# Kernel tuning notes

Hardware: AMD Instinct MI355X
Metric: run time of the kernel (lower is better)

## Reference

```python
import jax, jax.numpy as jnp
import numpy as np

N_QUBITS = 18
LAYERS = 6
DATA_REUPLOADING = True


def _apply_1q(state, gate, q, n):
    # state: [2^n] complex, gate: [2,2] complex, acts on qubit q (big-endian)
    s = state.reshape(2 ** q, 2, 2 ** (n - q - 1))
    s = jnp.einsum('ab,ibj->iaj', gate, s)
    return s.reshape(-1)


def _apply_cz_adj(state, q, n):
    # CZ on adjacent qubits (q, q+1): flip sign of |..11..> amplitudes
    s = state.reshape(2 ** q, 2, 2, 2 ** (n - q - 2))
    s = s.at[:, 1, 1, :].multiply(-1.0)
    return s.reshape(-1)


def _rx(t):
    c = jnp.cos(t / 2).astype(jnp.complex64)
    s = (-1j * jnp.sin(t / 2)).astype(jnp.complex64)
    return jnp.stack([jnp.stack([c, s]), jnp.stack([s, c])])


def _ry(t):
    c = jnp.cos(t / 2).astype(jnp.complex64)
    s = jnp.sin(t / 2).astype(jnp.complex64)
    return jnp.stack([jnp.stack([c, -s]), jnp.stack([s, c])])


def _rz(t):
    em = jnp.exp(-1j * t.astype(jnp.complex64) / 2)
    ep = jnp.exp(1j * t.astype(jnp.complex64) / 2)
    z = jnp.zeros((), jnp.complex64)
    return jnp.stack([jnp.stack([em, z]), jnp.stack([z, ep])])


def _circuit(x, input_scaling, variational):
    # Hardware-efficient ansatz: RX(data) encoding, RY+RZ variational, CZ chain
    n = N_QUBITS
    state = jnp.zeros(2 ** n, jnp.complex64).at[0].set(1.0)
    for l in range(LAYERS):
        if l == 0 or DATA_REUPLOADING:
            for q in range(n):
                state = _apply_1q(state, _rx(input_scaling[l, q] * x[q]), q, n)
        for q in range(n):
            state = _apply_1q(state, _ry(variational[l, q]), q, n)
        for q in range(n):
            state = _apply_1q(state, _rz(variational[l, n + q]), q, n)
        for q in range(n - 1):
            state = _apply_cz_adj(state, q, n)
    return state


def setup_inputs() -> dict:
    key = jax.random.key(0)
    k1, k2, k3 = jax.random.split(key, 3)
    x1 = jax.random.normal(k1, (N_QUBITS,), jnp.float32)
    x2 = jax.random.normal(k2, (N_QUBITS,), jnp.float32)
    input_scaling = jnp.ones((LAYERS, N_QUBITS), jnp.float32)
    variational = (jax.random.uniform(k3, (LAYERS, 2 * N_QUBITS), jnp.float32)
                   * 2 * np.pi - np.pi)
    return {"x1": x1, "x2": x2, "input_scaling": input_scaling,
            "variational": variational}


def reference(x1, x2, input_scaling, variational):
    psi1 = _circuit(x1, input_scaling, variational)
    psi2 = _circuit(x2, input_scaling, variational)
    # projector |0><0| expectation of U(x2)^dagger U(x1)|0> == |<psi2|psi1>|^2
    ov = jnp.vdot(psi2, psi1)
    return (ov.real ** 2 + ov.imag ** 2).astype(jnp.float32)
```

## Files before the change

### kernel.cpp

```cpp
#include <hip/hip_runtime.h>
#include <math.h>


#define NQ      18
#define NSTATE  (1 << NQ)
#define TPB     256
#define MAGIC   0x5EED5EEDu

__device__ __forceinline__ int SW(int i) { return i ^ ((i >> 5) & 31); }

__device__ __forceinline__ float2 cmulf(float2 a, float2 b) {
    return make_float2(a.x * b.x - a.y * b.y, a.x * b.y + a.y * b.x);
}

__device__ __forceinline__ float lxor(float x, int j) {
    if (j == 0) {
        int v = __float_as_int(x);
        return __int_as_float(__builtin_amdgcn_update_dpp(v, v, 0xB1, 0xF, 0xF, false));
    }
    if (j == 1) {
        int v = __float_as_int(x);
        return __int_as_float(__builtin_amdgcn_update_dpp(v, v, 0x4E, 0xF, 0xF, false));
    }
    return __shfl_xor(x, 1 << j, 64);
}

__device__ __forceinline__ void cpair(
    float& a0r, float& a0i, float& a1r, float& a1i,
    float u00r, float u00i, float u01r, float u01i,
    float u10r, float u10i, float u11r, float u11i)
{
    float n0r = u00r * a0r - u00i * a0i + u01r * a1r - u01i * a1i;
    float n0i = u00r * a0i + u00i * a0r + u01r * a1i + u01i * a1r;
    float n1r = u10r * a0r - u10i * a0i + u11r * a1r - u11i * a1i;
    float n1i = u10r * a0i + u10i * a0r + u11r * a1i + u11i * a1r;
    a0r = n0r; a0i = n0i; a1r = n1r; a1i = n1i;
}

template<int RB>
__device__ __forceinline__ void reg_gate8(float (&ar)[8], float (&ai)[8],
                                          const float2* up)
{
    float u00r = up[0].x, u00i = up[0].y, u01r = up[1].x, u01i = up[1].y;
    float u10r = up[2].x, u10i = up[2].y, u11r = up[3].x, u11i = up[3].y;
#pragma unroll
    for (int r = 0; r < 8; ++r) {
        if (r & RB) continue;
        int r1 = r | RB;
        cpair(ar[r], ai[r], ar[r1], ai[r1],
              u00r, u00i, u01r, u01i, u10r, u10i, u11r, u11i);
    }
}

__device__ __forceinline__ void lane_gate8(float (&ar)[8], float (&ai)[8],
                                           const float2* up, int lane, int j)
{
    float u00r = up[0].x, u00i = up[0].y, u01r = up[1].x, u01i = up[1].y;
    float u10r = up[2].x, u10i = up[2].y, u11r = up[3].x, u11i = up[3].y;
    int side = (lane >> j) & 1;
    float car = side ? u11r : u00r, cai = side ? u11i : u00i;
    float cbr = side ? u10r : u01r, cbi = side ? u10i : u01i;
#pragma unroll
    for (int r = 0; r < 8; ++r) {
        float pr = lxor(ar[r], j);
        float pi = lxor(ai[r], j);
        float mr = ar[r], mi = ai[r];
        ar[r] = car * mr - cai * mi + cbr * pr - cbi * pi;
        ai[r] = car * mi + cai * mr + cbr * pi + cbi * pr;
    }
}

__global__ __launch_bounds__(TPB) void sim_kernel(
    float2* __restrict__ states,
    const float* __restrict__ x1, const float* __restrict__ x2,
    const float* __restrict__ iscale, const float* __restrict__ var,
    double* __restrict__ acc, unsigned* __restrict__ cnt,
    unsigned* __restrict__ flags, float* __restrict__ out)
{
    __shared__ float sre[2048], sim_[2048];
    __shared__ float2 sUa[5 * 11 * 4];
    __shared__ float2 sUb[5 * 11 * 4];
    __shared__ float2 sDa[6 * 4];
    __shared__ float2 sDb[11 * 4];
    __shared__ double wr[4], wi[4];

    int blk = blockIdx.x, t = threadIdx.x, lane = t & 63, wave = t >> 6;
    int c = blk >> 7, gc = blk & 127;
    const float* xv = c ? x2 : x1;

    if (blk == 0 && t == 0) {
        acc[0] = 0.0; acc[1] = 0.0; *cnt = 0u;
        __hip_atomic_store(&flags[128 * 16], MAGIC, __ATOMIC_RELEASE,
                           __HIP_MEMORY_SCOPE_AGENT);
    }

    if (t < 110) {
        int which = t >= 55;
        int tt = which ? t - 55 : t;
        int l = tt / 11, w = tt % 11;
        int q = which ? (17 - w) : (10 - w);
        float tx = iscale[l * NQ + q] * xv[q];
        float ty = var[l * 2 * NQ + q];
        float tz = var[l * 2 * NQ + NQ + q];
        float sx, cx, sy, cy, sz, cz;
        sincosf(tx * 0.5f, &sx, &cx);
        sincosf(ty * 0.5f, &sy, &cy);
        sincosf(tz * 0.5f, &sz, &cz);
        float m00r = cy * cx,  m00i =  sy * sx;
        float m01r = -sy * cx, m01i = -cy * sx;
        float m10r = sy * cx,  m10i = -cy * sx;
        float m11r = cy * cx,  m11i = -sy * sx;
        float2* up = which ? &sUb[(l * 11 + w) * 4] : &sUa[(l * 11 + w) * 4];
        up[0] = make_float2(m00r * cz + m00i * sz, m00i * cz - m00r * sz);
        up[1] = make_float2(m01r * cz + m01i * sz, m01i * cz - m01r * sz);
        up[2] = make_float2(m10r * cz - m10i * sz, m10i * cz + m10r * sz);
        up[3] = make_float2(m11r * cz - m11i * sz, m11i * cz + m11r * sz);
    } else if (t < 127) {
        int isb = t >= 116;
        int j = isb ? (t - 116) : (t - 110);
        int q = isb ? (17 - j) : (5 - j);
        float d = iscale[5 * NQ + q] * (x1[q] - x2[q]);
        float sn, cs;
        sincosf(d * 0.5f, &sn, &cs);
        float2* up = isb ? &sDb[j * 4] : &sDa[j * 4];
        up[0] = make_float2(cs, 0.f);  up[1] = make_float2(0.f, sn);
        up[2] = make_float2(0.f, sn);  up[3] = make_float2(cs, 0.f);
    }
    __syncthreads();

    float ar[8], ai[8];
    auto W1 = [&](int r) { return r | (wave << 3) | (lane << 5); };
    auto W2 = [&](int r) { return wave | (r << 2) | (lane << 5); };
    auto X1 = [&](int r) { return lane | (wave << 6) | (r << 8); };
    auto X2 = [&](int r) { return lane | (r << 6) | (wave << 9); };
    auto rot = [&](auto from, auto to) {
#pragma unroll
        for (int r = 0; r < 8; ++r) { int s = SW(from(r)); sre[s] = ar[r]; sim_[s] = ai[r]; }
        __syncthreads();
#pragma unroll
        for (int r = 0; r < 8; ++r) { int s = SW(to(r)); ar[r] = sre[s]; ai[r] = sim_[s]; }
    };
    auto Ua = [&](int l, int w) -> const float2* { return &sUa[(l * 11 + w) * 4]; };
    auto Ub = [&](int l, int w) -> const float2* { return &sUb[(l * 11 + w) * 4]; };
    auto czfold = [&](unsigned M, auto gidx) {
#pragma unroll
        for (int r = 0; r < 8; ++r) {
            int i = gidx(r);
            if (__popc(i & (i >> 1) & M) & 1) { ar[r] = -ar[r]; ai[r] = -ai[r]; }
        }
    };
    auto g1_1 = [&](int r) { return W1(r) << 7; };
    auto g1_2 = [&](int r) { return W2(r) << 7; };
    auto g2_1 = [&](int r) { return (gc << 11) | X1(r); };
    auto g2_2 = [&](int r) { return (gc << 11) | X2(r); };

    {
        float2 com = make_float2(1.f, 0.f);
        const float2* u3 = Ua(0, 3); com = cmulf(com, (wave & 1) ? u3[2] : u3[0]);
        const float2* u4 = Ua(0, 4); com = cmulf(com, (wave >> 1) ? u4[2] : u4[0]);
#pragma unroll
        for (int j = 0; j < 6; ++j) {
            const float2* u = Ua(0, 5 + j);
            com = cmulf(com, ((lane >> j) & 1) ? u[2] : u[0]);
        }
        const float2* u0 = Ua(0, 0); const float2* u1 = Ua(0, 1); const float2* u2 = Ua(0, 2);
#pragma unroll
        for (int r = 0; r < 8; ++r) {
            float2 f = cmulf((r & 1) ? u0[2] : u0[0], (r & 2) ? u1[2] : u1[0]);
            f = cmulf(f, (r & 4) ? u2[2] : u2[0]);
            f = cmulf(com, f);
            ar[r] = f.x; ai[r] = f.y;
        }
    }
    czfold(0x1FF80u, g1_1);
    reg_gate8<2>(ar, ai, Ua(1, 1));
    reg_gate8<4>(ar, ai, Ua(1, 2));
#pragma unroll
    for (int j = 0; j < 6; ++j) lane_gate8(ar, ai, Ua(1, 5 + j), lane, j);
    rot(W1, W2);
    reg_gate8<2>(ar, ai, Ua(1, 3));
    reg_gate8<4>(ar, ai, Ua(1, 4));
    czfold(0x1FF00u, g1_2);
    reg_gate8<1>(ar, ai, Ua(2, 2));
    reg_gate8<2>(ar, ai, Ua(2, 3));
    reg_gate8<4>(ar, ai, Ua(2, 4));
#pragma unroll
    for (int j = 0; j < 6; ++j) lane_gate8(ar, ai, Ua(2, 5 + j), lane, j);
    rot(W2, W1);
    czfold(0x1FE00u, g1_1);
#pragma unroll
    for (int j = 0; j < 6; ++j) lane_gate8(ar, ai, Ua(3, 5 + j), lane, j);
    rot(W1, W2);
    reg_gate8<2>(ar, ai, Ua(3, 3));
    reg_gate8<4>(ar, ai, Ua(3, 4));
    czfold(0x1FC00u, g1_2);
    reg_gate8<4>(ar, ai, Ua(4, 4));
#pragma unroll
    for (int j = 0; j < 6; ++j) lane_gate8(ar, ai, Ua(4, 5 + j), lane, j);
    rot(W2, W1);
    czfold(0x1F800u, g1_1);
    if (c == 1) {
#pragma unroll
        for (int j = 0; j < 6; ++j) lane_gate8(ar, ai, &sDa[j * 4], lane, j);
    }
#pragma unroll
    for (int r = 0; r < 8; ++r) { int s = SW(W1(r)); sre[s] = ar[r]; sim_[s] = ai[r]; }
    __syncthreads();
#pragma unroll
    for (int r = 0; r < 8; ++r) {
        int x = X1(r);
        if ((x & 127) == 0) {
            int Wv = (gc << 4) | (x >> 7);
            int s = SW(Wv);
            ar[r] = sre[s]; ai[r] = sim_[s];
        } else { ar[r] = 0.f; ai[r] = 0.f; }
    }
    __syncthreads();

#pragma unroll
    for (int j = 0; j < 6; ++j) lane_gate8(ar, ai, Ub(0, j), lane, j);
    rot(X1, X2);
    reg_gate8<1>(ar, ai, Ub(0, 6));
    czfold(0x7Fu, g2_2);
#pragma unroll
    for (int j = 0; j < 6; ++j) lane_gate8(ar, ai, Ub(1, j), lane, j);
    reg_gate8<1>(ar, ai, Ub(1, 6));
    reg_gate8<2>(ar, ai, Ub(1, 7));
    rot(X2, X1);
    czfold(0xFFu, g2_1);
#pragma unroll
    for (int j = 0; j < 6; ++j) lane_gate8(ar, ai, Ub(2, j), lane, j);
    reg_gate8<1>(ar, ai, Ub(2, 8));
    rot(X1, X2);
    reg_gate8<1>(ar, ai, Ub(2, 6));
    reg_gate8<2>(ar, ai, Ub(2, 7));
    czfold(0x1FFu, g2_2);
#pragma unroll
    for (int j = 0; j < 6; ++j) lane_gate8(ar, ai, Ub(3, j), lane, j);
    reg_gate8<1>(ar, ai, Ub(3, 6));
    reg_gate8<2>(ar, ai, Ub(3, 7));
    reg_gate8<4>(ar, ai, Ub(3, 8));
    rot(X2, X1);
    reg_gate8<2>(ar, ai, Ub(3, 9));
    czfold(0x3FFu, g2_1);
#pragma unroll
    for (int j = 0; j < 6; ++j) lane_gate8(ar, ai, Ub(4, j), lane, j);
    reg_gate8<1>(ar, ai, Ub(4, 8));
    reg_gate8<2>(ar, ai, Ub(4, 9));
    reg_gate8<4>(ar, ai, Ub(4, 10));
    czfold(0x71Fu, g2_1);
    if (c == 1) {
#pragma unroll
        for (int j = 0; j < 5; ++j) lane_gate8(ar, ai, &sDb[j * 4], lane, j);
        reg_gate8<2>(ar, ai, &sDb[9 * 4]);
        reg_gate8<4>(ar, ai, &sDb[10 * 4]);
    }
    rot(X1, X2);
    reg_gate8<1>(ar, ai, Ub(4, 6));
    reg_gate8<2>(ar, ai, Ub(4, 7));
    czfold(0xE0u, g2_2);

    if (c == 0) {
#pragma unroll
        for (int r = 0; r < 8; ++r) {
            int i = (gc << 11) | X2(r);
            states[i] = make_float2(ar[r], ai[r]);
        }
        __syncthreads();
        if (t == 0) {
            __hip_atomic_store(&flags[gc * 16], MAGIC, __ATOMIC_RELEASE,
                               __HIP_MEMORY_SCOPE_AGENT);
        }
    } else {
        lane_gate8(ar, ai, &sDb[5 * 4], lane, 5);
        reg_gate8<1>(ar, ai, &sDb[6 * 4]);
        reg_gate8<2>(ar, ai, &sDb[7 * 4]);
        reg_gate8<4>(ar, ai, &sDb[8 * 4]);

        float d6 = iscale[5 * NQ + 6] * (x1[6] - x2[6]);
        float sn6, cs6;
        sincosf(d6 * 0.5f, &sn6, &cs6);
        float cf = cs6, sf = sn6;

        if (t == 0) {
            while (__hip_atomic_load(&flags[gc * 16], __ATOMIC_RELAXED,
                                     __HIP_MEMORY_SCOPE_AGENT) != MAGIC)
                __builtin_amdgcn_s_sleep(1);
            while (__hip_atomic_load(&flags[(gc ^ 1) * 16], __ATOMIC_RELAXED,
                                     __HIP_MEMORY_SCOPE_AGENT) != MAGIC)
                __builtin_amdgcn_s_sleep(1);
            while (__hip_atomic_load(&flags[128 * 16], __ATOMIC_RELAXED,
                                     __HIP_MEMORY_SCOPE_AGENT) != MAGIC)
                __builtin_amdgcn_s_sleep(1);
            __builtin_amdgcn_fence(__ATOMIC_ACQUIRE, "agent");
        }
        __syncthreads();

        double accr = 0.0, acci = 0.0;
#pragma unroll
        for (int r = 0; r < 8; ++r) {
            int i = (gc << 11) | X2(r);
            float2 p1 = states[i];
            float2 pp = states[i ^ 2048];
            float gr = cf * p1.x + sf * pp.y;
            float gi = cf * p1.y - sf * pp.x;
            accr += (double)ar[r] * gr + (double)ai[r] * gi;
            acci += (double)ar[r] * gi - (double)ai[r] * gr;
        }
        for (int o = 32; o > 0; o >>= 1) {
            accr += __shfl_down(accr, o, 64);
            acci += __shfl_down(acci, o, 64);
        }
        if (lane == 0) { wr[wave] = accr; wi[wave] = acci; }
        __syncthreads();
        if (t == 0) {
            double br = wr[0] + wr[1] + wr[2] + wr[3];
            double bi = wi[0] + wi[1] + wi[2] + wi[3];
            atomicAdd(&acc[0], br);
            atomicAdd(&acc[1], bi);
            __threadfence();
            unsigned old = atomicAdd(cnt, 1u);
            if (old == 127u) {
                double fr = atomicAdd(&acc[0], 0.0);
                double fi = atomicAdd(&acc[1], 0.0);
                out[0] = (float)(fr * fr + fi * fi);
            }
        }
    }
}

extern "C" void kernel_launch(void* const* d_in, const int* in_sizes, int n_in,
                              void* d_out, int out_size, void* d_ws, size_t ws_size,
                              hipStream_t stream)
{
    const float* x1 = (const float*)d_in[0];
    const float* x2 = (const float*)d_in[1];
    const float* iscale = (const float*)d_in[2];
    const float* var = (const float*)d_in[3];
    float* out = (float*)d_out;

    double*   acc    = (double*)((char*)d_ws + 8192);
    unsigned* cnt    = (unsigned*)((char*)d_ws + 8320);
    unsigned* flags  = (unsigned*)((char*)d_ws + 16384);
    float2*   states = (float2*)((char*)d_ws + 65536);

    sim_kernel<<<256, TPB, 0, stream>>>(states, x1, x2, iscale, var,
                                        acc, cnt, flags, out);
}
```

Measured before the change: 93.06 us.

## Double threads per block, halving per-thread register amplitudes

Raises block size from 256 to 512 threads so each thread holds 4 amplitudes instead of 8. The register-index and wave-bit mappings are redesigned, and the gate schedule and LDS rotations are reordered to suit the new layouts. A second barrier is added inside each rotation, and extra rotations are inserted near the end. The aim is more parallelism and latency hiding per block on a fixed grid of 256 blocks, at the cost of more barriers and LDS traffic per amplitude.

```diff
diff --git a/kernel.cpp b/kernel.cpp
--- a/kernel.cpp
+++ b/kernel.cpp
@@ -4,7 +4,7 @@
 
 #define NQ      18
 #define NSTATE  (1 << NQ)
-#define TPB     256
+#define TPB     512
 #define MAGIC   0x5EED5EEDu
 
 __device__ __forceinline__ int SW(int i) { return i ^ ((i >> 5) & 31); }
@@ -38,13 +38,13 @@
 }
 
 template<int RB>
-__device__ __forceinline__ void reg_gate8(float (&ar)[8], float (&ai)[8],
+__device__ __forceinline__ void reg_gate4(float (&ar)[4], float (&ai)[4],
                                           const float2* up)
 {
     float u00r = up[0].x, u00i = up[0].y, u01r = up[1].x, u01i = up[1].y;
     float u10r = up[2].x, u10i = up[2].y, u11r = up[3].x, u11i = up[3].y;
 #pragma unroll
-    for (int r = 0; r < 8; ++r) {
+    for (int r = 0; r < 4; ++r) {
         if (r & RB) continue;
         int r1 = r | RB;
         cpair(ar[r], ai[r], ar[r1], ai[r1],
@@ -52,7 +52,7 @@
     }
 }
 
-__device__ __forceinline__ void lane_gate8(float (&ar)[8], float (&ai)[8],
+__device__ __forceinline__ void lane_gate4(float (&ar)[4], float (&ai)[4],
                                            const float2* up, int lane, int j)
 {
     float u00r = up[0].x, u00i = up[0].y, u01r = up[1].x, u01i = up[1].y;
@@ -61,7 +61,7 @@
     float car = side ? u11r : u00r, cai = side ? u11i : u00i;
     float cbr = side ? u10r : u01r, cbi = side ? u10i : u01i;
 #pragma unroll
-    for (int r = 0; r < 8; ++r) {
+    for (int r = 0; r < 4; ++r) {
         float pr = lxor(ar[r], j);
         float pi = lxor(ai[r], j);
         float mr = ar[r], mi = ai[r];
@@ -82,10 +82,11 @@
     __shared__ float2 sUb[5 * 11 * 4];
     __shared__ float2 sDa[6 * 4];
     __shared__ float2 sDb[11 * 4];
-    __shared__ double wr[4], wi[4];
+    __shared__ double wr[8], wi[8];
 
     int blk = blockIdx.x, t = threadIdx.x, lane = t & 63, wave = t >> 6;
     int c = blk >> 7, gc = blk & 127;
+    int wv0 = wave & 1, wv1 = (wave >> 1) & 1, wv2 = (wave >> 2) & 1;
     const float* xv = c ? x2 : x1;
 
     if (blk == 0 && t == 0) {
@@ -128,87 +129,100 @@
     }
     __syncthreads();
 
-    float ar[8], ai[8];
-    auto W1 = [&](int r) { return r | (wave << 3) | (lane << 5); };
-    auto W2 = [&](int r) { return wave | (r << 2) | (lane << 5); };
-    auto X1 = [&](int r) { return lane | (wave << 6) | (r << 8); };
-    auto X2 = [&](int r) { return lane | (r << 6) | (wave << 9); };
+    float ar[4], ai[4];
+    auto V1 = [&](int r) { return wv0 | ((r & 1) << 1) | (((r >> 1) & 1) << 2)
+                                | (wv1 << 3) | (wv2 << 4) | (lane << 5); };
+    auto V2 = [&](int r) { return wv0 | (wv1 << 1) | (wv2 << 2)
+                                | ((r & 1) << 3) | (((r >> 1) & 1) << 4) | (lane << 5); };
+    auto V3 = [&](int r) { return wv0 | (wv1 << 1) | ((r & 1) << 2)
+                                | (((r >> 1) & 1) << 3) | (wv2 << 4) | (lane << 5); };
+    auto T1 = [&](int r) { return lane | ((r & 1) << 6) | (((r >> 1) & 1) << 7)
+                                | (wv0 << 8) | (wv1 << 9) | (wv2 << 10); };
+    auto T2 = [&](int r) { return lane | (wv0 << 6) | (wv1 << 7)
+                                | ((r & 1) << 8) | (((r >> 1) & 1) << 9) | (wv2 << 10); };
+    auto T6 = [&](int r) { return lane | (wv0 << 6) | (wv1 << 7) | (wv2 << 8)
+                                | ((r & 1) << 9) | (((r >> 1) & 1) << 10); };
+    auto T8 = [&](int r) { return lane | (wv0 << 6) | (wv1 << 7)
+                                | ((r & 1) << 8) | (wv2 << 9) | (((r >> 1) & 1) << 10); };
     auto rot = [&](auto from, auto to) {
 #pragma unroll
-        for (int r = 0; r < 8; ++r) { int s = SW(from(r)); sre[s] = ar[r]; sim_[s] = ai[r]; }
-        __syncthreads();
-#pragma unroll
-        for (int r = 0; r < 8; ++r) { int s = SW(to(r)); ar[r] = sre[s]; ai[r] = sim_[s]; }
+        for (int r = 0; r < 4; ++r) { int s = SW(from(r)); sre[s] = ar[r]; sim_[s] = ai[r]; }
+        __syncthreads();
+#pragma unroll
+        for (int r = 0; r < 4; ++r) { int s = SW(to(r)); ar[r] = sre[s]; ai[r] = sim_[s]; }
+        __syncthreads();
     };
     auto Ua = [&](int l, int w) -> const float2* { return &sUa[(l * 11 + w) * 4]; };
     auto Ub = [&](int l, int w) -> const float2* { return &sUb[(l * 11 + w) * 4]; };
     auto czfold = [&](unsigned M, auto gidx) {
 #pragma unroll
-        for (int r = 0; r < 8; ++r) {
+        for (int r = 0; r < 4; ++r) {
             int i = gidx(r);
             if (__popc(i & (i >> 1) & M) & 1) { ar[r] = -ar[r]; ai[r] = -ai[r]; }
         }
     };
-    auto g1_1 = [&](int r) { return W1(r) << 7; };
-    auto g1_2 = [&](int r) { return W2(r) << 7; };
-    auto g2_1 = [&](int r) { return (gc << 11) | X1(r); };
-    auto g2_2 = [&](int r) { return (gc << 11) | X2(r); };
+    auto gV1 = [&](int r) { return V1(r) << 7; };
+    auto gV2 = [&](int r) { return V2(r) << 7; };
+    auto gV3 = [&](int r) { return V3(r) << 7; };
+    auto gT1 = [&](int r) { return (gc << 11) | T1(r); };
+    auto gT2 = [&](int r) { return (gc << 11) | T2(r); };
+    auto gT6 = [&](int r) { return (gc << 11) | T6(r); };
 
     {
         float2 com = make_float2(1.f, 0.f);
-        const float2* u3 = Ua(0, 3); com = cmulf(com, (wave & 1) ? u3[2] : u3[0]);
-        const float2* u4 = Ua(0, 4); com = cmulf(com, (wave >> 1) ? u4[2] : u4[0]);
+        const float2* u0 = Ua(0, 0); com = cmulf(com, wv0 ? u0[2] : u0[0]);
+        const float2* u3 = Ua(0, 3); com = cmulf(com, wv1 ? u3[2] : u3[0]);
+        const float2* u4 = Ua(0, 4); com = cmulf(com, wv2 ? u4[2] : u4[0]);
 #pragma unroll
         for (int j = 0; j < 6; ++j) {
             const float2* u = Ua(0, 5 + j);
             com = cmulf(com, ((lane >> j) & 1) ? u[2] : u[0]);
         }
-        const float2* u0 = Ua(0, 0); const float2* u1 = Ua(0, 1); const float2* u2 = Ua(0, 2);
-#pragma unroll
-        for (int r = 0; r < 8; ++r) {
-            float2 f = cmulf((r & 1) ? u0[2] : u0[0], (r & 2) ? u1[2] : u1[0]);
-            f = cmulf(f, (r & 4) ? u2[2] : u2[0]);
+        const float2* u1 = Ua(0, 1); const float2* u2 = Ua(0, 2);
+#pragma unroll
+        for (int r = 0; r < 4; ++r) {
+            float2 f = cmulf((r & 1) ? u1[2] : u1[0], (r & 2) ? u2[2] : u2[0]);
             f = cmulf(com, f);
             ar[r] = f.x; ai[r] = f.y;
         }
     }
-    czfold(0x1FF80u, g1_1);
-    reg_gate8<2>(ar, ai, Ua(1, 1));
-    reg_gate8<4>(ar, ai, Ua(1, 2));
-#pragma unroll
-    for (int j = 0; j < 6; ++j) lane_gate8(ar, ai, Ua(1, 5 + j), lane, j);
-    rot(W1, W2);
-    reg_gate8<2>(ar, ai, Ua(1, 3));
-    reg_gate8<4>(ar, ai, Ua(1, 4));
-    czfold(0x1FF00u, g1_2);
-    reg_gate8<1>(ar, ai, Ua(2, 2));
-    reg_gate8<2>(ar, ai, Ua(2, 3));
-    reg_gate8<4>(ar, ai, Ua(2, 4));
-#pragma unroll
-    for (int j = 0; j < 6; ++j) lane_gate8(ar, ai, Ua(2, 5 + j), lane, j);
-    rot(W2, W1);
-    czfold(0x1FE00u, g1_1);
-#pragma unroll
-    for (int j = 0; j < 6; ++j) lane_gate8(ar, ai, Ua(3, 5 + j), lane, j);
-    rot(W1, W2);
-    reg_gate8<2>(ar, ai, Ua(3, 3));
-    reg_gate8<4>(ar, ai, Ua(3, 4));
-    czfold(0x1FC00u, g1_2);
-    reg_gate8<4>(ar, ai, Ua(4, 4));
-#pragma unroll
-    for (int j = 0; j < 6; ++j) lane_gate8(ar, ai, Ua(4, 5 + j), lane, j);
-    rot(W2, W1);
-    czfold(0x1F800u, g1_1);
+    czfold(0x1FF80u, gV1);
+    reg_gate4<1>(ar, ai, Ua(1, 1));
+    reg_gate4<2>(ar, ai, Ua(1, 2));
+#pragma unroll
+    for (int j = 0; j < 6; ++j) lane_gate4(ar, ai, Ua(1, 5 + j), lane, j);
+    rot(V1, V2);
+    reg_gate4<1>(ar, ai, Ua(1, 3));
+    reg_gate4<2>(ar, ai, Ua(1, 4));
+    czfold(0x1FF00u, gV2);
+    reg_gate4<1>(ar, ai, Ua(2, 3));
+    reg_gate4<2>(ar, ai, Ua(2, 4));
+#pragma unroll
+    for (int j = 0; j < 6; ++j) lane_gate4(ar, ai, Ua(2, 5 + j), lane, j);
+    rot(V2, V3);
+    reg_gate4<1>(ar, ai, Ua(2, 2));
+    czfold(0x1FE00u, gV3);
+    reg_gate4<2>(ar, ai, Ua(3, 3));
+#pragma unroll
+    for (int j = 0; j < 6; ++j) lane_gate4(ar, ai, Ua(3, 5 + j), lane, j);
+    rot(V3, V2);
+    reg_gate4<2>(ar, ai, Ua(3, 4));
+    czfold(0x1FC00u, gV2);
+    reg_gate4<2>(ar, ai, Ua(4, 4));
+#pragma unroll
+    for (int j = 0; j < 6; ++j) lane_gate4(ar, ai, Ua(4, 5 + j), lane, j);
+    rot(V2, V1);
+    czfold(0x1F800u, gV1);
     if (c == 1) {
 #pragma unroll
-        for (int j = 0; j < 6; ++j) lane_gate8(ar, ai, &sDa[j * 4], lane, j);
-    }
-#pragma unroll
-    for (int r = 0; r < 8; ++r) { int s = SW(W1(r)); sre[s] = ar[r]; sim_[s] = ai[r]; }
+        for (int j = 0; j < 6; ++j) lane_gate4(ar, ai, &sDa[j * 4], lane, j);
+    }
+#pragma unroll
+    for (int r = 0; r < 4; ++r) { int s = SW(V1(r)); sre[s] = ar[r]; sim_[s] = ai[r]; }
     __syncthreads();
 #pragma unroll
-    for (int r = 0; r < 8; ++r) {
-        int x = X1(r);
+    for (int r = 0; r < 4; ++r) {
+        int x = T1(r);
         if ((x & 127) == 0) {
             int Wv = (gc << 4) | (x >> 7);
             int s = SW(Wv);
@@ -218,52 +232,46 @@
     __syncthreads();
 
 #pragma unroll
-    for (int j = 0; j < 6; ++j) lane_gate8(ar, ai, Ub(0, j), lane, j);
-    rot(X1, X2);
-    reg_gate8<1>(ar, ai, Ub(0, 6));
-    czfold(0x7Fu, g2_2);
-#pragma unroll
-    for (int j = 0; j < 6; ++j) lane_gate8(ar, ai, Ub(1, j), lane, j);
-    reg_gate8<1>(ar, ai, Ub(1, 6));
-    reg_gate8<2>(ar, ai, Ub(1, 7));
-    rot(X2, X1);
-    czfold(0xFFu, g2_1);
-#pragma unroll
-    for (int j = 0; j < 6; ++j) lane_gate8(ar, ai, Ub(2, j), lane, j);
-    reg_gate8<1>(ar, ai, Ub(2, 8));
-    rot(X1, X2);
-    reg_gate8<1>(ar, ai, Ub(2, 6));
-    reg_gate8<2>(ar, ai, Ub(2, 7));
-    czfold(0x1FFu, g2_2);
-#pragma unroll
-    for (int j = 0; j < 6; ++j) lane_gate8(ar, ai, Ub(3, j), lane, j);
-    reg_gate8<1>(ar, ai, Ub(3, 6));
-    reg_gate8<2>(ar, ai, Ub(3, 7));
-    reg_gate8<4>(ar, ai, Ub(3, 8));
-    rot(X2, X1);
-    reg_gate8<2>(ar, ai, Ub(3, 9));
-    czfold(0x3FFu, g2_1);
-#pragma unroll
-    for (int j = 0; j < 6; ++j) lane_gate8(ar, ai, Ub(4, j), lane, j);
-    reg_gate8<1>(ar, ai, Ub(4, 8));
-    reg_gate8<2>(ar, ai, Ub(4, 9));
-    reg_gate8<4>(ar, ai, Ub(4, 10));
-    czfold(0x71Fu, g2_1);
-    if (c == 1) {
-#pragma unroll
-        for (int j = 0; j < 5; ++j) lane_gate8(ar, ai, &sDb[j * 4], lane, j);
-        reg_gate8<2>(ar, ai, &sDb[9 * 4]);
-        reg_gate8<4>(ar, ai, &sDb[10 * 4]);
-    }
-    rot(X1, X2);
-    reg_gate8<1>(ar, ai, Ub(4, 6));
-    reg_gate8<2>(ar, ai, Ub(4, 7));
-    czfold(0xE0u, g2_2);
+    for (int j = 0; j < 6; ++j) lane_gate4(ar, ai, Ub(0, j), lane, j);
+    reg_gate4<1>(ar, ai, Ub(0, 6));
+    czfold(0x7Fu, gT1);
+#pragma unroll
+    for (int j = 0; j < 6; ++j) lane_gate4(ar, ai, Ub(1, j), lane, j);
+    reg_gate4<1>(ar, ai, Ub(1, 6));
+    reg_gate4<2>(ar, ai, Ub(1, 7));
+    rot(T1, T2);
+    czfold(0xFFu, gT2);
+#pragma unroll
+    for (int j = 0; j < 6; ++j) lane_gate4(ar, ai, Ub(2, j), lane, j);
+    reg_gate4<1>(ar, ai, Ub(2, 8));
+    rot(T2, T1);
+    reg_gate4<1>(ar, ai, Ub(2, 6));
+    reg_gate4<2>(ar, ai, Ub(2, 7));
+    czfold(0x1FFu, gT1);
+#pragma unroll
+    for (int j = 0; j < 6; ++j) lane_gate4(ar, ai, Ub(3, j), lane, j);
+    reg_gate4<1>(ar, ai, Ub(3, 6));
+    reg_gate4<2>(ar, ai, Ub(3, 7));
+    rot(T1, T2);
+    reg_gate4<1>(ar, ai, Ub(3, 8));
+    reg_gate4<2>(ar, ai, Ub(3, 9));
+    czfold(0x3FFu, gT2);
+#pragma unroll
+    for (int j = 0; j < 6; ++j) lane_gate4(ar, ai, Ub(4, j), lane, j);
+    reg_gate4<1>(ar, ai, Ub(4, 8));
+    reg_gate4<2>(ar, ai, Ub(4, 9));
+    rot(T2, T1);
+    reg_gate4<1>(ar, ai, Ub(4, 6));
+    reg_gate4<2>(ar, ai, Ub(4, 7));
+    czfold(0xE0u, gT1);
+    rot(T1, T6);
+    reg_gate4<2>(ar, ai, Ub(4, 10));
+    czfold(0x71Fu, gT6);
 
     if (c == 0) {
 #pragma unroll
-        for (int r = 0; r < 8; ++r) {
-            int i = (gc << 11) | X2(r);
+        for (int r = 0; r < 4; ++r) {
+            int i = (gc << 11) | T6(r);
             states[i] = make_float2(ar[r], ai[r]);
         }
         __syncthreads();
@@ -272,10 +280,16 @@
                                __HIP_MEMORY_SCOPE_AGENT);
         }
     } else {
-        lane_gate8(ar, ai, &sDb[5 * 4], lane, 5);
-        reg_gate8<1>(ar, ai, &sDb[6 * 4]);
-        reg_gate8<2>(ar, ai, &sDb[7 * 4]);
-        reg_gate8<4>(ar, ai, &sDb[8 * 4]);
+#pragma unroll
+        for (int j = 0; j < 5; ++j) lane_gate4(ar, ai, &sDb[j * 4], lane, j);
+        reg_gate4<1>(ar, ai, &sDb[9 * 4]);
+        reg_gate4<2>(ar, ai, &sDb[10 * 4]);
+        rot(T6, T1);
+        lane_gate4(ar, ai, &sDb[5 * 4], lane, 5);
+        reg_gate4<1>(ar, ai, &sDb[6 * 4]);
+        reg_gate4<2>(ar, ai, &sDb[7 * 4]);
+        rot(T1, T8);
+        reg_gate4<1>(ar, ai, &sDb[8 * 4]);
 
         float d6 = iscale[5 * NQ + 6] * (x1[6] - x2[6]);
         float sn6, cs6;
@@ -298,8 +312,8 @@
 
         double accr = 0.0, acci = 0.0;
 #pragma unroll
-        for (int r = 0; r < 8; ++r) {
-            int i = (gc << 11) | X2(r);
+        for (int r = 0; r < 4; ++r) {
+            int i = (gc << 11) | T8(r);
             float2 p1 = states[i];
             float2 pp = states[i ^ 2048];
             float gr = cf * p1.x + sf * pp.y;
@@ -314,8 +328,9 @@
         if (lane == 0) { wr[wave] = accr; wi[wave] = acci; }
         __syncthreads();
         if (t == 0) {
-            double br = wr[0] + wr[1] + wr[2] + wr[3];
-            double bi = wi[0] + wi[1] + wi[2] + wi[3];
+            double br = 0.0, bi = 0.0;
+#pragma unroll
+            for (int w = 0; w < 8; ++w) { br += wr[w]; bi += wi[w]; }
             atomicAdd(&acc[0], br);
             atomicAdd(&acc[1], bi);
             __threadfence();
```

New measurement: 84.94 us. 1.1x faster.
